# Kernel tuning notes

Hardware: AMD Instinct MI355X
Metric: run time of the kernel (lower is better)

The kernel has to match this reference:

```python
import jax, jax.numpy as jnp
import numpy as np

NUM_HEADS = 16
KEY_DIM = 64
B, S, D = 2, 2048, 1024


def setup_inputs() -> dict:
    key = jax.random.key(0)
    ks = jax.random.split(key, 5)
    scale = 1.0 / np.sqrt(D)
    return {
        "x": jax.random.normal(ks[0], (B, S, D), dtype=jnp.float32),
        "Wq": jax.random.normal(ks[1], (D, NUM_HEADS * KEY_DIM), dtype=jnp.float32) * scale,
        "Wk": jax.random.normal(ks[2], (D, NUM_HEADS * KEY_DIM), dtype=jnp.float32) * scale,
        "Wv": jax.random.normal(ks[3], (D, NUM_HEADS * KEY_DIM), dtype=jnp.float32) * scale,
        "Wo": jax.random.normal(ks[4], (NUM_HEADS * KEY_DIM, D), dtype=jnp.float32) * scale,
    }


def reference(x, Wq, Wk, Wv, Wo):
    b, s, d = x.shape
    h, kd = NUM_HEADS, KEY_DIM
    # QKV projections -> [B, H, S, Kd]
    q = (x @ Wq).reshape(b, s, h, kd).transpose(0, 2, 1, 3)
    k = (x @ Wk).reshape(b, s, h, kd).transpose(0, 2, 1, 3)
    v = (x @ Wv).reshape(b, s, h, kd).transpose(0, 2, 1, 3)
    # scaled dot-product attention, full [B,H,S,S] scores (faithful to source)
    logits = jnp.einsum("bhqd,bhkd->bhqk", q, k) / jnp.sqrt(jnp.float32(kd))
    attn = jax.nn.softmax(logits, axis=-1)
    out = jnp.einsum("bhqk,bhkd->bhqd", attn, v)  # [B,H,S,Kd]
    out = out.transpose(0, 2, 1, 3).reshape(b, s, h * kd)
    return out @ Wo
```

## Files before the change

### kernel.cpp

```cpp
#include <hip/hip_runtime.h>


typedef __attribute__((ext_vector_type(8))) short short8;
typedef __attribute__((ext_vector_type(4))) float f32x4;

#define M_ROWS 4096
#define N_COLS 1024
#define K_DIM  1024
#define SEQ    2048

#define QSCALE 0.18033688011111772f

#if defined(__has_builtin)
#if __has_builtin(__builtin_amdgcn_exp2f)
#define EXP2(x) __builtin_amdgcn_exp2f(x)
#endif
#endif
#ifndef EXP2
#define EXP2(x) exp2f(x)
#endif

#define WAITCNT_VM8 0x0F78
#define WAITCNT_VM4 0x0F74

__device__ inline unsigned short f2bf(float f) {
  unsigned int u = __float_as_uint(f);
  u += 0x7fffu + ((u >> 16) & 1u);
  return (unsigned short)(u >> 16);
}

__device__ inline unsigned int cvtpk(float lo, float hi) {
  unsigned int r;
  asm("v_cvt_pk_bf16_f32 %0, %1, %2" : "=v"(r) : "v"(lo), "v"(hi));
  return r;
}

__device__ inline void swap32(unsigned int& a, unsigned int& b) {
  asm("v_permlane32_swap_b32 %0, %1" : "+v"(a), "+v"(b));
}
__device__ inline void swap16(unsigned int& a, unsigned int& b) {
  asm("v_permlane16_swap_b32 %0, %1" : "+v"(a), "+v"(b));
}

__device__ inline void async_load16(const unsigned short* gptr, unsigned short* lptr) {
  __builtin_amdgcn_global_load_lds(
      (const __attribute__((address_space(1))) unsigned int*)gptr,
      (__attribute__((address_space(3))) unsigned int*)lptr, 16, 0, 0);
}

__device__ inline int wave_is_bf16(const unsigned short* __restrict__ x) {
  const int lane = threadIdx.x & 63;
  int bad = 0;
#pragma unroll
  for (int i = 0; i < 16; ++i) {
    float f = __uint_as_float((unsigned int)x[lane + i * 64] << 16);
    if (!(fabsf(f) < 1e4f)) bad = 1;
  }
  return __any(bad) ? 0 : 1;
}

__global__ __launch_bounds__(256) void convert_all_kernel(
    const void* __restrict__ xsrc,
    const void* __restrict__ s0, const void* __restrict__ s1,
    const void* __restrict__ s2, const void* __restrict__ s3,
    unsigned short* __restrict__ xb,
    unsigned short* __restrict__ d0, unsigned short* __restrict__ d1,
    unsigned short* __restrict__ d2, unsigned short* __restrict__ d3) {
  __shared__ unsigned short t[32][33];
  const int z = blockIdx.z;
  const int isbf = wave_is_bf16((const unsigned short*)xsrc);
  const int tid = threadIdx.x;

  if (z == 4) {
    const int n4 = (M_ROWS * K_DIM) / 4;
    const int start = (blockIdx.y * 32 + blockIdx.x) * 256 + tid;
    const int stride = 1024 * 256;
    for (int i = start; i < n4; i += stride) {
      if (isbf) {
        ((uint2*)xb)[i] = ((const uint2*)xsrc)[i];
      } else {
        float4 v = ((const float4*)xsrc)[i];
        ushort4 o;
        o.x = f2bf(v.x); o.y = f2bf(v.y); o.z = f2bf(v.z); o.w = f2bf(v.w);
        ((ushort4*)xb)[i] = o;
      }
    }
    return;
  }

  const void* src = (z == 0) ? s0 : (z == 1) ? s1 : (z == 2) ? s2 : s3;
  unsigned short* dst = (z == 0) ? d0 : (z == 1) ? d1 : (z == 2) ? d2 : d3;
  const int r0 = blockIdx.y * 32, c0 = blockIdx.x * 32;
  const int kr = tid >> 3, nc = (tid & 7) * 4;
  if (isbf) {
    const unsigned short* W = (const unsigned short*)src;
    uint2 v = *(const uint2*)(W + (size_t)(r0 + kr) * K_DIM + c0 + nc);
    t[kr][nc] = v.x & 0xffff; t[kr][nc + 1] = v.x >> 16;
    t[kr][nc + 2] = v.y & 0xffff; t[kr][nc + 3] = v.y >> 16;
  } else {
    const float* W = (const float*)src;
    float4 v = *(const float4*)(W + (size_t)(r0 + kr) * K_DIM + c0 + nc);
    t[kr][nc] = f2bf(v.x); t[kr][nc + 1] = f2bf(v.y);
    t[kr][nc + 2] = f2bf(v.z); t[kr][nc + 3] = f2bf(v.w);
  }
  __syncthreads();
  const int nr = tid >> 3, kc = (tid & 7) * 4;
  uint2 w;
  w.x = (unsigned int)t[kc][nr] | ((unsigned int)t[kc + 1][nr] << 16);
  w.y = (unsigned int)t[kc + 2][nr] | ((unsigned int)t[kc + 3][nr] << 16);
  *(uint2*)(dst + (size_t)(c0 + nr) * K_DIM + r0 + kc) = w;
}

#define GEMM_DMA(Aptr, Bptr, KTOT, KB, BUF)                                       \
  _Pragma("unroll") for (int r = 0; r < 2; ++r) {                                 \
    int s = r * 256 + wave * 64 + lane;                                           \
    int row = s >> 2, c = s & 3;                                                  \
    int g = c ^ ((row ^ (row >> 2)) & 3);                                         \
    async_load16((Aptr) + (size_t)(m0 + row) * (KTOT) + (KB) + g * 8,             \
                 &As[BUF][(size_t)(r * 256 + wave * 64) * 8]);                    \
    async_load16((Bptr) + (size_t)(n0 + row) * (KTOT) + (KB) + g * 8,             \
                 &Bs[BUF][(size_t)(r * 256 + wave * 64) * 8]);                    \
  }

#define GEMM_MAIN_LOOP(Aptr, Bptr, KTOT)                                          \
  f32x4 acc[4][4];                                                                \
  _Pragma("unroll") for (int i = 0; i < 4; ++i)                                   \
  _Pragma("unroll") for (int j = 0; j < 4; ++j)                                   \
      acc[i][j] = (f32x4){0.f, 0.f, 0.f, 0.f};                                    \
  const int xr = (l15 ^ (l15 >> 2)) & 3;                                          \
  GEMM_DMA(Aptr, Bptr, KTOT, 0, 0)                                                \
  GEMM_DMA(Aptr, Bptr, KTOT, 32, 1)                                               \
  int cur = 0;                                                                    \
  for (int kb = 0; kb < (KTOT); kb += 32) {                                       \
    __builtin_amdgcn_s_waitcnt(WAITCNT_VM4);                                      \
    __syncthreads();                                                              \
    const int kb2 = (kb + 64) & ((KTOT) - 1);                                     \
    const int nx2 = (cur == 0) ? 2 : (cur - 1);                    \
    GEMM_DMA(Aptr, Bptr, KTOT, kb2, nx2)                                          \
    short8 am[4], bn[4];                                                          \
    _Pragma("unroll") for (int i = 0; i < 4; ++i) {                               \
      int arow = wr * 64 + i * 16 + l15;                                          \
      int brow = wc * 64 + i * 16 + l15;                                          \
      int cc = quad ^ xr;                                                         \
      am[i] = *(const short8*)(&As[cur][arow * 32 + cc * 8]);                     \
      bn[i] = *(const short8*)(&Bs[cur][brow * 32 + cc * 8]);                     \
    }                                                                             \
    _Pragma("unroll") for (int i = 0; i < 4; ++i)                                 \
    _Pragma("unroll") for (int j = 0; j < 4; ++j)                                 \
        acc[i][j] = __builtin_amdgcn_mfma_f32_16x16x32_bf16(am[i], bn[j],         \
                                                            acc[i][j], 0, 0, 0); \
    cur = (cur == 2) ? 0 : cur + 1;                                               \
  }

__global__ __launch_bounds__(256, 3) void qkv_gemm_kernel(
    const unsigned short* __restrict__ Xb,
    const unsigned short* __restrict__ Wqt,
    const unsigned short* __restrict__ Wkt,
    const unsigned short* __restrict__ Wvt,
    unsigned short* __restrict__ Qb,
    unsigned short* __restrict__ Kb,
    unsigned short* __restrict__ Vt) {
  __shared__ __align__(16) unsigned short As[3][128 * 32];
  __shared__ __align__(16) unsigned short Bs[3][128 * 32];
  const int tid = threadIdx.x;
  const int wave = tid >> 6, lane = tid & 63;
  const int quad = lane >> 4, l15 = lane & 15;
  const int wr = wave >> 1, wc = wave & 1;
  const int m0 = blockIdx.x * 128;
  const int n0 = blockIdx.y * 128;
  const int wsel = blockIdx.z;
  const unsigned short* __restrict__ Bt =
      (wsel == 0) ? Wqt : ((wsel == 1) ? Wkt : Wvt);

  GEMM_MAIN_LOOP(Xb, Bt, K_DIM)

#pragma unroll
  for (int i = 0; i < 4; ++i) {
#pragma unroll
    for (int j = 0; j < 4; ++j) {
      int mbase = m0 + wr * 64 + i * 16 + quad * 4;
      int n = n0 + wc * 64 + j * 16 + l15;
      int h = n >> 6, d = n & 63;
      if (wsel == 2) {
        int b_ = mbase >> 11, s = mbase & 2047;
        uint2 w;
        w.x = cvtpk(acc[i][j][0], acc[i][j][1]);
        w.y = cvtpk(acc[i][j][2], acc[i][j][3]);
        *(uint2*)(Vt + ((size_t)(b_ * 16 + h) * 64 + d) * SEQ + s) = w;
      } else {
#pragma unroll
        for (int r = 0; r < 4; ++r) {
          int m = mbase + r;
          int b_ = m >> 11, s = m & 2047;
          float val = acc[i][j][r];
          if (wsel == 0)
            Qb[((size_t)(b_ * 16 + h) * SEQ + s) * 64 + d] = f2bf(val * QSCALE);
          else
            Kb[((size_t)(b_ * 16 + h) * SEQ + s) * 64 + d] = f2bf(val);
        }
      }
    }
  }
}

__global__ __launch_bounds__(256, 2) void flash_kernel(
    const unsigned short* __restrict__ Qb,
    const unsigned short* __restrict__ Kb,
    const unsigned short* __restrict__ Vt,
    unsigned short* __restrict__ Ob) {
  __shared__ __align__(16) unsigned short Klds[2][128 * 64];
  __shared__ __align__(16) unsigned short Vlds[2][64 * 128];
  const int tid = threadIdx.x;
  const int wave = tid >> 6, lane = tid & 63;
  const int quad = lane >> 4, l15 = lane & 15;
  const int gid = blockIdx.x;
  const int bh = gid & 31;
  const int qidx = gid >> 5;
  const int qbase = qidx * 128 + wave * 32;

  const unsigned short* __restrict__ Qp = Qb + (size_t)bh * SEQ * 64;
  const unsigned short* __restrict__ Kp = Kb + (size_t)bh * SEQ * 64;
  const unsigned short* __restrict__ Vp = Vt + (size_t)bh * 64 * SEQ;

  short8 qf[2][2];
#pragma unroll
  for (int g = 0; g < 2; ++g)
#pragma unroll
    for (int h = 0; h < 2; ++h)
      qf[g][h] = *(const short8*)(Qp + (size_t)(qbase + g * 16 + l15) * 64 + h * 32 + quad * 8);

  f32x4 O[2][4];
#pragma unroll
  for (int g = 0; g < 2; ++g)
#pragma unroll
    for (int t = 0; t < 4; ++t) O[g][t] = (f32x4){0.f, 0.f, 0.f, 0.f};
  float l_i[2] = {0.f, 0.f};

#define FLASH_DMA(KB, BUF)                                                     \
  _Pragma("unroll") for (int r = 0; r < 4; ++r) {                              \
    int s = r * 256 + tid;                                                     \
    int krow = s >> 3, kc = s & 7;                                             \
    int kg = kc ^ (krow & 7);                                                  \
    async_load16(Kp + (size_t)((KB) + krow) * 64 + kg * 8,                     \
                 &Klds[BUF][(size_t)(r * 256 + wave * 64) * 8]);               \
    int vrow = s >> 4, vc = s & 15;                                            \
    int vg = vc ^ (vrow & 15);                                                 \
    async_load16(Vp + (size_t)vrow * SEQ + (KB) + vg * 8,                      \
                 &Vlds[BUF][(size_t)(r * 256 + wave * 64) * 8]);               \
  }

#define QK_READ(t)                                                             \
  int row = (t) * 16 + l15;                                                    \
  int c0 = quad ^ (row & 7), c1 = (quad + 4) ^ (row & 7);                      \
  short8 k0 = *(const short8*)(&Klds[p][row * 64 + c0 * 8]);                   \
  short8 k1 = *(const short8*)(&Klds[p][row * 64 + c1 * 8]);

#define SOFTMAX_G(SRC, PB, G)                                                  \
  {                                                                            \
    float rs = 0.f;                                                            \
    unsigned int wx[8], wy[8];                                                 \
    _Pragma("unroll") for (int t = 0; t < 8; ++t) {                            \
      float p0 = EXP2(SRC[t][0]);                                              \
      float p1 = EXP2(SRC[t][1]);                                              \
      float p2 = EXP2(SRC[t][2]);                                              \
      float p3 = EXP2(SRC[t][3]);                                              \
      rs += (p0 + p1) + (p2 + p3);                                             \
      wx[t] = cvtpk(p0, p1);                                                   \
      wy[t] = cvtpk(p2, p3);                                                   \
    }                                                                          \
    l_i[G] += rs;                                                              \
    _Pragma("unroll") for (int m = 0; m < 4; ++m) {                            \
      unsigned int a = wx[2 * m], c = wx[2 * m + 1];                           \
      unsigned int b = wy[2 * m], d = wy[2 * m + 1];                           \
      swap32(a, c); swap16(a, c);                \
      swap32(b, d); swap16(b, d);                \
      union { short8 s; unsigned int u[4]; } P;                                \
      P.u[0] = a; P.u[1] = b; P.u[2] = c; P.u[3] = d;                          \
      PB[m] = P.s;                                                             \
    }                                                                          \
  }

#define PV_G(PB, G)                                                            \
  _Pragma("unroll") for (int td = 0; td < 4; ++td) {                           \
    int vrow = td * 16 + l15;                                                  \
    _Pragma("unroll") for (int m = 0; m < 4; ++m) {                            \
      short8 vf = *(const short8*)(&Vlds[p][vrow * 128 +                       \
                                           (((m * 4 + quad) ^ l15) * 8)]);     \
      O[G][td] = __builtin_amdgcn_mfma_f32_16x16x32_bf16(vf, PB[m],            \
                                                         O[G][td], 0, 0, 0);   \
    }                                                                          \
  }

  FLASH_DMA(0, 0)

  for (int kb = 0; kb < SEQ; kb += 128) {
    const int p = (kb >> 7) & 1;
    const int kbn = (kb + 128) & (SEQ - 1);
    FLASH_DMA(kbn, p ^ 1)
    __builtin_amdgcn_s_waitcnt(WAITCNT_VM8);
    __syncthreads();

    f32x4 sT0[8], sT1[8];
    __builtin_amdgcn_s_setprio(1);
#pragma unroll
    for (int t = 0; t < 8; ++t) {
      QK_READ(t)
      sT0[t] = __builtin_amdgcn_mfma_f32_16x16x32_bf16(k0, qf[0][0],
               (f32x4){0.f, 0.f, 0.f, 0.f}, 0, 0, 0);
      sT0[t] = __builtin_amdgcn_mfma_f32_16x16x32_bf16(k1, qf[0][1], sT0[t], 0, 0, 0);
    }
    __builtin_amdgcn_s_setprio(0);

#pragma unroll
    for (int t = 0; t < 8; ++t) {
      QK_READ(t)
      sT1[t] = __builtin_amdgcn_mfma_f32_16x16x32_bf16(k0, qf[1][0],
               (f32x4){0.f, 0.f, 0.f, 0.f}, 0, 0, 0);
      sT1[t] = __builtin_amdgcn_mfma_f32_16x16x32_bf16(k1, qf[1][1], sT1[t], 0, 0, 0);
    }
    short8 pb0[4];
    SOFTMAX_G(sT0, pb0, 0)

    PV_G(pb0, 0)
    short8 pb1[4];
    SOFTMAX_G(sT1, pb1, 1)

    PV_G(pb1, 1)

    __syncthreads();
  }

#pragma unroll
  for (int g = 0; g < 2; ++g) {
    l_i[g] += __shfl_xor(l_i[g], 16);
    l_i[g] += __shfl_xor(l_i[g], 32);
  }

  const int b_ = bh >> 4, h = bh & 15;
#pragma unroll
  for (int g = 0; g < 2; ++g) {
    const float inv = 1.f / l_i[g];
    unsigned short* orow = Ob + ((size_t)(b_ * SEQ) + qbase + g * 16 + l15) * N_COLS + h * 64;
#pragma unroll
    for (int t = 0; t < 4; ++t) {
      uint2 w;
      w.x = cvtpk(O[g][t][0] * inv, O[g][t][1] * inv);
      w.y = cvtpk(O[g][t][2] * inv, O[g][t][3] * inv);
      *(uint2*)(orow + t * 16 + quad * 4) = w;
    }
  }
#undef FLASH_DMA
#undef QK_READ
#undef SOFTMAX_G
#undef PV_G
}

__global__ __launch_bounds__(256, 3) void out_gemm_kernel(
    const unsigned short* __restrict__ Ob,
    const unsigned short* __restrict__ Wot,
    void* __restrict__ out,
    const unsigned short* __restrict__ xdet) {
  __shared__ __align__(16) unsigned short As[3][128 * 32];
  __shared__ __align__(16) unsigned short Bs[3][128 * 32];
  const int tid = threadIdx.x;
  const int wave = tid >> 6, lane = tid & 63;
  const int quad = lane >> 4, l15 = lane & 15;
  const int wr = wave >> 1, wc = wave & 1;
  const int m0 = blockIdx.x * 128;
  const int n0 = blockIdx.y * 128;
  const int isbf = wave_is_bf16(xdet);

  GEMM_MAIN_LOOP(Ob, Wot, N_COLS)

#pragma unroll
  for (int i = 0; i < 4; ++i) {
#pragma unroll
    for (int j = 0; j < 4; ++j) {
      int mbase = m0 + wr * 64 + i * 16 + quad * 4;
      int n = n0 + wc * 64 + j * 16 + l15;
#pragma unroll
      for (int r = 0; r < 4; ++r) {
        float val = acc[i][j][r];
        if (isbf) ((unsigned short*)out)[(size_t)(mbase + r) * K_DIM + n] = f2bf(val);
        else      ((float*)out)[(size_t)(mbase + r) * K_DIM + n] = val;
      }
    }
  }
}

extern "C" void kernel_launch(void* const* d_in, const int* in_sizes, int n_in,
                              void* d_out, int out_size, void* d_ws, size_t ws_size,
                              hipStream_t stream) {
  const void* x  = d_in[0];
  const void* wq = d_in[1];
  const void* wk = d_in[2];
  const void* wv = d_in[3];
  const void* wo = d_in[4];

  char* ws = (char*)d_ws;
  size_t off = 0;
  unsigned short* xb  = (unsigned short*)(ws + off); off += (size_t)M_ROWS * K_DIM * 2;
  unsigned short* wqt = (unsigned short*)(ws + off); off += (size_t)K_DIM * N_COLS * 2;
  unsigned short* wkt = (unsigned short*)(ws + off); off += (size_t)K_DIM * N_COLS * 2;
  unsigned short* wvt = (unsigned short*)(ws + off); off += (size_t)K_DIM * N_COLS * 2;
  unsigned short* wot = (unsigned short*)(ws + off); off += (size_t)N_COLS * K_DIM * 2;
  unsigned short* Qb  = (unsigned short*)(ws + off); off += (size_t)M_ROWS * 1024 * 2;
  unsigned short* Kb  = (unsigned short*)(ws + off); off += (size_t)M_ROWS * 1024 * 2;
  unsigned short* Vtb = (unsigned short*)(ws + off); off += (size_t)M_ROWS * 1024 * 2;
  unsigned short* Ob  = (unsigned short*)(ws + off); off += (size_t)M_ROWS * N_COLS * 2;
  (void)ws_size; (void)in_sizes; (void)n_in; (void)out_size;

  convert_all_kernel<<<dim3(32, 32, 5), 256, 0, stream>>>(x, wq, wk, wv, wo,
                                                          xb, wqt, wkt, wvt, wot);
  qkv_gemm_kernel<<<dim3(32, 8, 3), 256, 0, stream>>>(xb, wqt, wkt, wvt, Qb, Kb, Vtb);
  flash_kernel<<<512, 256, 0, stream>>>(Qb, Kb, Vtb, Ob);
  out_gemm_kernel<<<dim3(32, 8), 256, 0, stream>>>(Ob, wot, d_out,
                                                   (const unsigned short*)x);
}
```

Baseline: 191.0 us.

## Load flash K/V directly from global and double-buffer GEMM pipeline

The flash attention kernel stops staging K and V tiles in LDS through async copies and barriers. Each wave now reads its K and V fragments straight from global memory into registers and interleaves the two query groups' MFMAs. This removes LDS traffic and block-wide syncs, but every wave re-reads the same K/V data from global or cache without reuse. Separately, the GEMM kernels go from a triple-buffered LDS prefetch to double buffering with an extra barrier per k-step, which lowers LDS use but shortens how far loads run ahead of compute.

```diff
diff --git a/kernel.cpp b/kernel.cpp
--- a/kernel.cpp
+++ b/kernel.cpp
@@ -20,7 +20,6 @@
 #define EXP2(x) exp2f(x)
 #endif
 
-#define WAITCNT_VM8 0x0F78
 #define WAITCNT_VM4 0x0F74
 
 __device__ inline unsigned short f2bf(float f) {
@@ -129,27 +128,25 @@
       acc[i][j] = (f32x4){0.f, 0.f, 0.f, 0.f};                                    \
   const int xr = (l15 ^ (l15 >> 2)) & 3;                                          \
   GEMM_DMA(Aptr, Bptr, KTOT, 0, 0)                                                \
-  GEMM_DMA(Aptr, Bptr, KTOT, 32, 1)                                               \
-  int cur = 0;                                                                    \
   for (int kb = 0; kb < (KTOT); kb += 32) {                                       \
+    const int pp = (kb >> 5) & 1;                                                 \
+    const int kbn = (kb + 32) & ((KTOT) - 1);                                     \
+    GEMM_DMA(Aptr, Bptr, KTOT, kbn, pp ^ 1)                                       \
     __builtin_amdgcn_s_waitcnt(WAITCNT_VM4);                                      \
     __syncthreads();                                                              \
-    const int kb2 = (kb + 64) & ((KTOT) - 1);                                     \
-    const int nx2 = (cur == 0) ? 2 : (cur - 1);                    \
-    GEMM_DMA(Aptr, Bptr, KTOT, kb2, nx2)                                          \
     short8 am[4], bn[4];                                                          \
     _Pragma("unroll") for (int i = 0; i < 4; ++i) {                               \
       int arow = wr * 64 + i * 16 + l15;                                          \
       int brow = wc * 64 + i * 16 + l15;                                          \
       int cc = quad ^ xr;                                                         \
-      am[i] = *(const short8*)(&As[cur][arow * 32 + cc * 8]);                     \
-      bn[i] = *(const short8*)(&Bs[cur][brow * 32 + cc * 8]);                     \
+      am[i] = *(const short8*)(&As[pp][arow * 32 + cc * 8]);                      \
+      bn[i] = *(const short8*)(&Bs[pp][brow * 32 + cc * 8]);                      \
     }                                                                             \
     _Pragma("unroll") for (int i = 0; i < 4; ++i)                                 \
     _Pragma("unroll") for (int j = 0; j < 4; ++j)                                 \
         acc[i][j] = __builtin_amdgcn_mfma_f32_16x16x32_bf16(am[i], bn[j],         \
                                                             acc[i][j], 0, 0, 0); \
-    cur = (cur == 2) ? 0 : cur + 1;                                               \
+    __syncthreads();                                                              \
   }
 
 __global__ __launch_bounds__(256, 3) void qkv_gemm_kernel(
@@ -160,8 +157,8 @@
     unsigned short* __restrict__ Qb,
     unsigned short* __restrict__ Kb,
     unsigned short* __restrict__ Vt) {
-  __shared__ __align__(16) unsigned short As[3][128 * 32];
-  __shared__ __align__(16) unsigned short Bs[3][128 * 32];
+  __shared__ __align__(16) unsigned short As[2][128 * 32];
+  __shared__ __align__(16) unsigned short Bs[2][128 * 32];
   const int tid = threadIdx.x;
   const int wave = tid >> 6, lane = tid & 63;
   const int quad = lane >> 4, l15 = lane & 15;
@@ -208,8 +205,6 @@
     const unsigned short* __restrict__ Kb,
     const unsigned short* __restrict__ Vt,
     unsigned short* __restrict__ Ob) {
-  __shared__ __align__(16) unsigned short Klds[2][128 * 64];
-  __shared__ __align__(16) unsigned short Vlds[2][64 * 128];
   const int tid = threadIdx.x;
   const int wave = tid >> 6, lane = tid & 63;
   const int quad = lane >> 4, l15 = lane & 15;
@@ -235,25 +230,6 @@
 #pragma unroll
     for (int t = 0; t < 4; ++t) O[g][t] = (f32x4){0.f, 0.f, 0.f, 0.f};
   float l_i[2] = {0.f, 0.f};
-
-#define FLASH_DMA(KB, BUF)                                                     \
-  _Pragma("unroll") for (int r = 0; r < 4; ++r) {                              \
-    int s = r * 256 + tid;                                                     \
-    int krow = s >> 3, kc = s & 7;                                             \
-    int kg = kc ^ (krow & 7);                                                  \
-    async_load16(Kp + (size_t)((KB) + krow) * 64 + kg * 8,                     \
-                 &Klds[BUF][(size_t)(r * 256 + wave * 64) * 8]);               \
-    int vrow = s >> 4, vc = s & 15;                                            \
-    int vg = vc ^ (vrow & 15);                                                 \
-    async_load16(Vp + (size_t)vrow * SEQ + (KB) + vg * 8,                      \
-                 &Vlds[BUF][(size_t)(r * 256 + wave * 64) * 8]);               \
-  }
-
-#define QK_READ(t)                                                             \
-  int row = (t) * 16 + l15;                                                    \
-  int c0 = quad ^ (row & 7), c1 = (quad + 4) ^ (row & 7);                      \
-  short8 k0 = *(const short8*)(&Klds[p][row * 64 + c0 * 8]);                   \
-  short8 k1 = *(const short8*)(&Klds[p][row * 64 + c1 * 8]);
 
 #define SOFTMAX_G(SRC, PB, G)                                                  \
   {                                                                            \
@@ -280,54 +256,39 @@
     }                                                                          \
   }
 
-#define PV_G(PB, G)                                                            \
-  _Pragma("unroll") for (int td = 0; td < 4; ++td) {                           \
-    int vrow = td * 16 + l15;                                                  \
-    _Pragma("unroll") for (int m = 0; m < 4; ++m) {                            \
-      short8 vf = *(const short8*)(&Vlds[p][vrow * 128 +                       \
-                                           (((m * 4 + quad) ^ l15) * 8)]);     \
-      O[G][td] = __builtin_amdgcn_mfma_f32_16x16x32_bf16(vf, PB[m],            \
-                                                         O[G][td], 0, 0, 0);   \
-    }                                                                          \
-  }
-
-  FLASH_DMA(0, 0)
-
   for (int kb = 0; kb < SEQ; kb += 128) {
-    const int p = (kb >> 7) & 1;
-    const int kbn = (kb + 128) & (SEQ - 1);
-    FLASH_DMA(kbn, p ^ 1)
-    __builtin_amdgcn_s_waitcnt(WAITCNT_VM8);
-    __syncthreads();
-
     f32x4 sT0[8], sT1[8];
     __builtin_amdgcn_s_setprio(1);
 #pragma unroll
     for (int t = 0; t < 8; ++t) {
-      QK_READ(t)
+      const unsigned short* krow = Kp + (size_t)(kb + t * 16 + l15) * 64;
+      short8 k0 = *(const short8*)(krow + quad * 8);
+      short8 k1 = *(const short8*)(krow + 32 + quad * 8);
       sT0[t] = __builtin_amdgcn_mfma_f32_16x16x32_bf16(k0, qf[0][0],
                (f32x4){0.f, 0.f, 0.f, 0.f}, 0, 0, 0);
       sT0[t] = __builtin_amdgcn_mfma_f32_16x16x32_bf16(k1, qf[0][1], sT0[t], 0, 0, 0);
-    }
-    __builtin_amdgcn_s_setprio(0);
-
-#pragma unroll
-    for (int t = 0; t < 8; ++t) {
-      QK_READ(t)
       sT1[t] = __builtin_amdgcn_mfma_f32_16x16x32_bf16(k0, qf[1][0],
                (f32x4){0.f, 0.f, 0.f, 0.f}, 0, 0, 0);
       sT1[t] = __builtin_amdgcn_mfma_f32_16x16x32_bf16(k1, qf[1][1], sT1[t], 0, 0, 0);
     }
-    short8 pb0[4];
+    __builtin_amdgcn_s_setprio(0);
+
+    short8 pb0[4], pb1[4];
     SOFTMAX_G(sT0, pb0, 0)
-
-    PV_G(pb0, 0)
-    short8 pb1[4];
     SOFTMAX_G(sT1, pb1, 1)
 
-    PV_G(pb1, 1)
-
-    __syncthreads();
+    __builtin_amdgcn_s_setprio(1);
+#pragma unroll
+    for (int td = 0; td < 4; ++td) {
+      const unsigned short* vrow = Vp + (size_t)(td * 16 + l15) * SEQ + kb;
+#pragma unroll
+      for (int m = 0; m < 4; ++m) {
+        short8 vf = *(const short8*)(vrow + (m * 4 + quad) * 8);
+        O[0][td] = __builtin_amdgcn_mfma_f32_16x16x32_bf16(vf, pb0[m], O[0][td], 0, 0, 0);
+        O[1][td] = __builtin_amdgcn_mfma_f32_16x16x32_bf16(vf, pb1[m], O[1][td], 0, 0, 0);
+      }
+    }
+    __builtin_amdgcn_s_setprio(0);
   }
 
 #pragma unroll
@@ -349,10 +310,7 @@
       *(uint2*)(orow + t * 16 + quad * 4) = w;
     }
   }
-#undef FLASH_DMA
-#undef QK_READ
 #undef SOFTMAX_G
-#undef PV_G
 }
 
 __global__ __launch_bounds__(256, 3) void out_gemm_kernel(
@@ -360,8 +318,8 @@
     const unsigned short* __restrict__ Wot,
     void* __restrict__ out,
     const unsigned short* __restrict__ xdet) {
-  __shared__ __align__(16) unsigned short As[3][128 * 32];
-  __shared__ __align__(16) unsigned short Bs[3][128 * 32];
+  __shared__ __align__(16) unsigned short As[2][128 * 32];
+  __shared__ __align__(16) unsigned short Bs[2][128 * 32];
   const int tid = threadIdx.x;
   const int wave = tid >> 6, lane = tid & 63;
   const int quad = lane >> 4, l15 = lane & 15;
```

Result: slower. 255.7 us (+33.9%).

## Fuse Q/K/V projections into one 512-thread block sharing the X tile

Applied to the files above, without the earlier changes.

The QKV GEMM becomes one kernel per 128x128 output tile with 8 waves. It loads a single X tile and three weight tiles, computing Q, K and V together so X is fetched once instead of three times. The shared GEMM pipeline also moves from a 3-stage to a 2-stage double buffer with an extra barrier per iteration, which shrinks LDS use but exposes more load latency. The grid drops from 768 to 256 blocks at one block per CU, which lowers occupancy and latency hiding.

```diff
diff --git a/kernel.cpp b/kernel.cpp
--- a/kernel.cpp
+++ b/kernel.cpp
@@ -129,30 +129,28 @@
       acc[i][j] = (f32x4){0.f, 0.f, 0.f, 0.f};                                    \
   const int xr = (l15 ^ (l15 >> 2)) & 3;                                          \
   GEMM_DMA(Aptr, Bptr, KTOT, 0, 0)                                                \
-  GEMM_DMA(Aptr, Bptr, KTOT, 32, 1)                                               \
-  int cur = 0;                                                                    \
   for (int kb = 0; kb < (KTOT); kb += 32) {                                       \
+    const int pp = (kb >> 5) & 1;                                                 \
+    const int kbn = (kb + 32) & ((KTOT) - 1);                                     \
+    GEMM_DMA(Aptr, Bptr, KTOT, kbn, pp ^ 1)                                       \
     __builtin_amdgcn_s_waitcnt(WAITCNT_VM4);                                      \
     __syncthreads();                                                              \
-    const int kb2 = (kb + 64) & ((KTOT) - 1);                                     \
-    const int nx2 = (cur == 0) ? 2 : (cur - 1);                    \
-    GEMM_DMA(Aptr, Bptr, KTOT, kb2, nx2)                                          \
     short8 am[4], bn[4];                                                          \
     _Pragma("unroll") for (int i = 0; i < 4; ++i) {                               \
       int arow = wr * 64 + i * 16 + l15;                                          \
       int brow = wc * 64 + i * 16 + l15;                                          \
       int cc = quad ^ xr;                                                         \
-      am[i] = *(const short8*)(&As[cur][arow * 32 + cc * 8]);                     \
-      bn[i] = *(const short8*)(&Bs[cur][brow * 32 + cc * 8]);                     \
+      am[i] = *(const short8*)(&As[pp][arow * 32 + cc * 8]);                      \
+      bn[i] = *(const short8*)(&Bs[pp][brow * 32 + cc * 8]);                      \
     }                                                                             \
     _Pragma("unroll") for (int i = 0; i < 4; ++i)                                 \
     _Pragma("unroll") for (int j = 0; j < 4; ++j)                                 \
         acc[i][j] = __builtin_amdgcn_mfma_f32_16x16x32_bf16(am[i], bn[j],         \
                                                             acc[i][j], 0, 0, 0); \
-    cur = (cur == 2) ? 0 : cur + 1;                                               \
-  }
-
-__global__ __launch_bounds__(256, 3) void qkv_gemm_kernel(
+    __syncthreads();                                                              \
+  }
+
+__global__ __launch_bounds__(512, 1) void qkv_gemm_kernel(
     const unsigned short* __restrict__ Xb,
     const unsigned short* __restrict__ Wqt,
     const unsigned short* __restrict__ Wkt,
@@ -160,47 +158,94 @@
     unsigned short* __restrict__ Qb,
     unsigned short* __restrict__ Kb,
     unsigned short* __restrict__ Vt) {
-  __shared__ __align__(16) unsigned short As[3][128 * 32];
-  __shared__ __align__(16) unsigned short Bs[3][128 * 32];
+  __shared__ __align__(16) unsigned short As[2][128 * 32];
+  __shared__ __align__(16) unsigned short Bs[3][2][128 * 32];
   const int tid = threadIdx.x;
   const int wave = tid >> 6, lane = tid & 63;
   const int quad = lane >> 4, l15 = lane & 15;
-  const int wr = wave >> 1, wc = wave & 1;
+  const int wr = wave >> 2, wc = wave & 3;
   const int m0 = blockIdx.x * 128;
   const int n0 = blockIdx.y * 128;
-  const int wsel = blockIdx.z;
-  const unsigned short* __restrict__ Bt =
-      (wsel == 0) ? Wqt : ((wsel == 1) ? Wkt : Wvt);
-
-  GEMM_MAIN_LOOP(Xb, Bt, K_DIM)
+
+#define QKV_DMA(KB, BUF)                                                       \
+  {                                                                            \
+    int s = tid;                                                               \
+    int row = s >> 2, c = s & 3;                                               \
+    int g = c ^ ((row ^ (row >> 2)) & 3);                                      \
+    async_load16(Xb + (size_t)(m0 + row) * K_DIM + (KB) + g * 8,               \
+                 &As[BUF][(size_t)(wave * 64) * 8]);                           \
+    async_load16(Wqt + (size_t)(n0 + row) * K_DIM + (KB) + g * 8,              \
+                 &Bs[0][BUF][(size_t)(wave * 64) * 8]);                        \
+    async_load16(Wkt + (size_t)(n0 + row) * K_DIM + (KB) + g * 8,              \
+                 &Bs[1][BUF][(size_t)(wave * 64) * 8]);                        \
+    async_load16(Wvt + (size_t)(n0 + row) * K_DIM + (KB) + g * 8,              \
+                 &Bs[2][BUF][(size_t)(wave * 64) * 8]);                        \
+  }
+
+  f32x4 acc[3][4][2];
+#pragma unroll
+  for (int w3 = 0; w3 < 3; ++w3)
+#pragma unroll
+    for (int i = 0; i < 4; ++i)
+#pragma unroll
+      for (int j = 0; j < 2; ++j)
+        acc[w3][i][j] = (f32x4){0.f, 0.f, 0.f, 0.f};
+  const int xr = (l15 ^ (l15 >> 2)) & 3;
+
+  QKV_DMA(0, 0)
+  for (int kb = 0; kb < K_DIM; kb += 32) {
+    const int pp = (kb >> 5) & 1;
+    const int kbn = (kb + 32) & (K_DIM - 1);
+    QKV_DMA(kbn, pp ^ 1)
+    __builtin_amdgcn_s_waitcnt(WAITCNT_VM4);
+    __syncthreads();
+    const int cc = quad ^ xr;
+    short8 am[4], bn[3][2];
+#pragma unroll
+    for (int i = 0; i < 4; ++i) {
+      int arow = wr * 64 + i * 16 + l15;
+      am[i] = *(const short8*)(&As[pp][arow * 32 + cc * 8]);
+    }
+#pragma unroll
+    for (int w3 = 0; w3 < 3; ++w3)
+#pragma unroll
+      for (int j = 0; j < 2; ++j) {
+        int brow = wc * 32 + j * 16 + l15;
+        bn[w3][j] = *(const short8*)(&Bs[w3][pp][brow * 32 + cc * 8]);
+      }
+#pragma unroll
+    for (int w3 = 0; w3 < 3; ++w3)
+#pragma unroll
+      for (int i = 0; i < 4; ++i)
+#pragma unroll
+        for (int j = 0; j < 2; ++j)
+          acc[w3][i][j] = __builtin_amdgcn_mfma_f32_16x16x32_bf16(
+              am[i], bn[w3][j], acc[w3][i][j], 0, 0, 0);
+    __syncthreads();
+  }
 
 #pragma unroll
   for (int i = 0; i < 4; ++i) {
 #pragma unroll
-    for (int j = 0; j < 4; ++j) {
+    for (int j = 0; j < 2; ++j) {
       int mbase = m0 + wr * 64 + i * 16 + quad * 4;
-      int n = n0 + wc * 64 + j * 16 + l15;
+      int n = n0 + wc * 32 + j * 16 + l15;
       int h = n >> 6, d = n & 63;
-      if (wsel == 2) {
-        int b_ = mbase >> 11, s = mbase & 2047;
-        uint2 w;
-        w.x = cvtpk(acc[i][j][0], acc[i][j][1]);
-        w.y = cvtpk(acc[i][j][2], acc[i][j][3]);
-        *(uint2*)(Vt + ((size_t)(b_ * 16 + h) * 64 + d) * SEQ + s) = w;
-      } else {
-#pragma unroll
-        for (int r = 0; r < 4; ++r) {
-          int m = mbase + r;
-          int b_ = m >> 11, s = m & 2047;
-          float val = acc[i][j][r];
-          if (wsel == 0)
-            Qb[((size_t)(b_ * 16 + h) * SEQ + s) * 64 + d] = f2bf(val * QSCALE);
-          else
-            Kb[((size_t)(b_ * 16 + h) * SEQ + s) * 64 + d] = f2bf(val);
-        }
+      int b_ = mbase >> 11, s = mbase & 2047;
+      uint2 wv2;
+      wv2.x = cvtpk(acc[2][i][j][0], acc[2][i][j][1]);
+      wv2.y = cvtpk(acc[2][i][j][2], acc[2][i][j][3]);
+      *(uint2*)(Vt + ((size_t)(b_ * 16 + h) * 64 + d) * SEQ + s) = wv2;
+#pragma unroll
+      for (int r = 0; r < 4; ++r) {
+        int m = mbase + r;
+        int bb = m >> 11, ss = m & 2047;
+        Qb[((size_t)(bb * 16 + h) * SEQ + ss) * 64 + d] = f2bf(acc[0][i][j][r] * QSCALE);
+        Kb[((size_t)(bb * 16 + h) * SEQ + ss) * 64 + d] = f2bf(acc[1][i][j][r]);
       }
     }
   }
+#undef QKV_DMA
 }
 
 __global__ __launch_bounds__(256, 2) void flash_kernel(
@@ -360,8 +405,8 @@
     const unsigned short* __restrict__ Wot,
     void* __restrict__ out,
     const unsigned short* __restrict__ xdet) {
-  __shared__ __align__(16) unsigned short As[3][128 * 32];
-  __shared__ __align__(16) unsigned short Bs[3][128 * 32];
+  __shared__ __align__(16) unsigned short As[2][128 * 32];
+  __shared__ __align__(16) unsigned short Bs[2][128 * 32];
   const int tid = threadIdx.x;
   const int wave = tid >> 6, lane = tid & 63;
   const int quad = lane >> 4, l15 = lane & 15;
@@ -412,7 +457,7 @@
 
   convert_all_kernel<<<dim3(32, 32, 5), 256, 0, stream>>>(x, wq, wk, wv, wo,
                                                           xb, wqt, wkt, wvt, wot);
-  qkv_gemm_kernel<<<dim3(32, 8, 3), 256, 0, stream>>>(xb, wqt, wkt, wvt, Qb, Kb, Vtb);
+  qkv_gemm_kernel<<<dim3(32, 8), 512, 0, stream>>>(xb, wqt, wkt, wvt, Qb, Kb, Vtb);
   flash_kernel<<<512, 256, 0, stream>>>(Qb, Kb, Vtb, Ob);
   out_gemm_kernel<<<dim3(32, 8), 256, 0, stream>>>(Ob, wot, d_out,
                                                    (const unsigned short*)x);
```

Result: no change. 192.8 us (+0.9%).
